# Optimization experiments

Hardware: AMD Instinct MI355X
Metric: run time of the kernel (lower is better)

Reference implementation:

```python
import jax, jax.numpy as jnp
import numpy as np
from jax import lax

H, W = 14, 14          # spatial input_size
K = 6                  # mask_size (square)
ST = 2                 # mask_stride
_xs = np.arange(0, H - K + 1, ST)   # mask/window positions; (H-K)%ST==0 so grid matches avg_pool2d
M = len(_xs)
# pairwise rectangle-intersection coordinates between mask R1 (index a) and window W2 (index b)
_lo = np.maximum(_xs[:, None], _xs[None, :])                       # [M,M]
_hi = np.maximum(np.minimum(_xs[:, None] + K, _xs[None, :] + K), _lo)  # [M,M], clamped (empty -> zero area)


def setup_inputs() -> dict:
    key = jax.random.key(0)
    x = jax.random.normal(key, (32, 1000, H, W), dtype=jnp.float32)
    return {"x": x}


def _forward(x):
    B, C = x.shape[0], x.shape[1]
    total = jnp.sum(x, axis=(2, 3))  # [B,C]  == unmasked_logits
    # window sums == avg_pool2d(divisor_override=1); also equals sum over each mask region R1
    winsum = lax.reduce_window(x, 0.0, lax.add, (1, 1, K, K), (1, 1, ST, ST), 'VALID')  # [B,C,M,M]
    one_mask_logits = total[:, :, None, None] - winsum                # [B,C,M,M]
    one_mask_pred = jnp.argmax(one_mask_logits, axis=1)               # [B,M,M]
    pred = jnp.argmax(total, axis=1)                                  # [B]
    disagree = one_mask_pred != pred[:, None, None]                   # [B,M,M]

    # summed-area table for O(1) rectangle sums (zero-padded)
    sat = jnp.pad(jnp.cumsum(jnp.cumsum(x, axis=2), axis=3), ((0, 0), (0, 0), (1, 0), (1, 0)))
    xhi = _hi[:, None, :, None]; xlo = _lo[:, None, :, None]          # depend on (i, k)
    yhi = _hi[None, :, None, :]; ylo = _lo[None, :, None, :]          # depend on (j, l)
    # sum of x over R1(i,j) ∩ W2(k,l): [B,C,M,M,M,M]
    overlap = (sat[:, :, xhi, yhi] - sat[:, :, xlo, yhi]
               - sat[:, :, xhi, ylo] + sat[:, :, xlo, ylo])

    # two-mask logits: total - sum(R1) - sum(W2) + sum(R1 ∩ W2)
    two = (total[:, :, None, None, None, None]
           - winsum[:, :, :, :, None, None]
           - winsum[:, :, None, None, :, :]
           + overlap)                                                 # [B,C,M,M,M,M]
    two_pred = jnp.argmax(two, axis=1)                                # [B,M,M,M,M]

    # a disagreer (i,j) is confirmed if ALL second-mask preds equal its one-mask pred
    agree = jnp.all(two_pred == one_mask_pred[:, :, :, None, None], axis=(3, 4))  # [B,M,M]
    cand = (disagree & agree).reshape(B, -1)                          # row-major (i,j) order
    first = jnp.argmax(cand, axis=1)                                  # first confirmed disagreer
    new_pred = jnp.take_along_axis(one_mask_pred.reshape(B, -1), first[:, None], axis=1)[:, 0]
    pred = jnp.where(jnp.any(cand, axis=1), new_pred, pred)
    return pred, one_mask_logits


def reference(x):
    pred, _ = _forward(x)
    return pred
```

## Files before the change

kernel.cpp:

```cpp
#include <hip/hip_runtime.h>


#define NC 1000
#define NBC 32000
#define CHUNKS 4
#define CLEN 250
#define NG 14
#define MAXST 26

__host__ __device__ constexpr int tri_off(int p) { return p * 25 - p * (p - 1) / 2; }

__device__ __forceinline__ unsigned fkey(float v) {
    unsigned u = __float_as_uint(v);
    return u ^ (unsigned)(((int)u >> 31) | 0x80000000);
}

__global__ __launch_bounds__(256) void satA(const float* __restrict__ x,
                                            float* __restrict__ Sws) {
    __shared__ float lx[64 * 197];
    const int tid = threadIdx.x;
    const int blk = blockIdx.x;
    const float4* x4 = reinterpret_cast<const float4*>(x) + (size_t)blk * 3136;
#pragma unroll
    for (int it = 0; it < 13; ++it) {
        int f = it * 256 + tid;
        if (f < 3136) {
            float4 v = x4[f];
            int img = f / 49;
            int off = f - img * 49;
            float* d = &lx[img * 197 + off * 4];
            d[0] = v.x; d[1] = v.y; d[2] = v.z; d[3] = v.w;
        }
    }
    __syncthreads();
    if (tid < 64) {
        const float* im = &lx[tid * 197];
        float S[8][8];
#pragma unroll
        for (int c = 0; c < 8; ++c) S[0][c] = 0.f;
        float colacc[7];
#pragma unroll
        for (int c = 0; c < 7; ++c) colacc[c] = 0.f;
#pragma unroll
        for (int r = 0; r < 7; ++r) {
            float rowf[28];
#pragma unroll
            for (int j = 0; j < 28; ++j) rowf[j] = im[r * 28 + j];
            S[r + 1][0] = 0.f;
            float run = 0.f;
#pragma unroll
            for (int c = 0; c < 7; ++c) {
                float blk2 = rowf[2 * c] + rowf[2 * c + 1] + rowf[14 + 2 * c] + rowf[14 + 2 * c + 1];
                colacc[c] += blk2;
                run += colacc[c];
                S[r + 1][c + 1] = run;
            }
        }
        const int bc = blk * 64 + tid;
#pragma unroll
        for (int k = 0; k < 64; ++k)
            Sws[(size_t)k * NBC + bc] = S[k >> 3][k & 7];
    }
}

#define WSUM(i, j) (S[((i)+3)*8+((j)+3)] - S[(i)*8+((j)+3)] - S[((i)+3)*8+(j)] + S[(i)*8+(j)])

template <int G>
__device__ __forceinline__ void procB(const float* __restrict__ Sws, int b, int chunk,
                                      unsigned long long* __restrict__ part,
                                      unsigned* __restrict__ kv, unsigned* __restrict__ kc) {
    const int tid = threadIdx.x;
    const int c = chunk * CLEN + tid;
    const bool act = (tid < CLEN);

    float S[64];
    if (act) {
        const int base = b * NC + c;
#pragma unroll
        for (int k = 0; k < 64; ++k) S[k] = Sws[k * NBC + base];
    } else {
#pragma unroll
        for (int k = 0; k < 64; ++k) S[k] = 0.f;
    }
    const float total = S[63];
    constexpr int NST = (G == 13) ? 26 : 25;

#pragma unroll
    for (int ph = 0; ph < 2; ++ph) {
        const int lo = ph * 13;
        const int cnt = (NST - lo) < 13 ? (NST - lo) : 13;
        if (act) {
#pragma unroll
            for (int i = 0; i < 13; ++i) {
                const int sl = lo + i;
                if (sl < NST) {
                    float v;
                    if constexpr (G == 13) {
                        v = (sl < 25) ? (total - WSUM(sl / 5, sl % 5)) : total;
                    } else {
                        const int pid = G * 25 + sl;
                        int p = 0;
                        while (tri_off(p + 1) <= pid) ++p;
                        const int q = p + (pid - tri_off(p));
                        const int p1 = p / 5, p2 = p % 5, q1 = q / 5, q2 = q % 5;
                        const int rlo = (p1 > q1 ? p1 : q1);
                        const int rmn = (p1 < q1 ? p1 : q1);
                        const int rhi = (rmn + 3 > rlo ? rmn + 3 : rlo);
                        const int clo = (p2 > q2 ? p2 : q2);
                        const int cmn = (p2 < q2 ? p2 : q2);
                        const int chi = (cmn + 3 > clo ? cmn + 3 : clo);
                        const float rect = S[rhi * 8 + chi] - S[rlo * 8 + chi]
                                         - S[rhi * 8 + clo] + S[rlo * 8 + clo];
                        v = ((total - WSUM(p1, p2)) - WSUM(q1, q2)) + rect;
                    }
                    kv[tid * 13 + i] = fkey(v);
                    kc[tid * 13 + i] = ~(unsigned)c;
                }
            }
        } else {
#pragma unroll
            for (int i = 0; i < 13; ++i) { kv[tid * 13 + i] = 0u; kc[tid * 13 + i] = 0u; }
        }
        __syncthreads();
        if (tid < 208) {
            const int s = tid >> 4, seg = tid & 15;
            if (s < cnt) {
                unsigned bk = 0u, bc2 = 0u;
#pragma unroll
                for (int i = 0; i < 16; ++i) {
                    const int row = seg * 16 + i;
                    unsigned k2 = kv[row * 13 + s], c2 = kc[row * 13 + s];
                    if (k2 > bk || (k2 == bk && c2 > bc2)) { bk = k2; bc2 = c2; }
                }
#pragma unroll
                for (int off = 1; off < 16; off <<= 1) {
                    unsigned ok = __shfl_xor(bk, off, 16);
                    unsigned oc = __shfl_xor(bc2, off, 16);
                    if (ok > bk || (ok == bk && oc > bc2)) { bk = ok; bc2 = oc; }
                }
                if (seg == 0)
                    part[((b * NG + G) * CHUNKS + chunk) * MAXST + lo + s] =
                        ((unsigned long long)bk << 32) | bc2;
            }
        }
        __syncthreads();
    }
}

__global__ __launch_bounds__(256) void kernB(const float* __restrict__ Sws,
                                             unsigned long long* __restrict__ part) {
    __shared__ unsigned kv[256 * 13];
    __shared__ unsigned kc[256 * 13];
    const int b = blockIdx.x / 56;
    const int r = blockIdx.x % 56;
    const int g = r >> 2;
    const int chunk = r & 3;
#define CASE_G(T) case T: procB<T>(Sws, b, chunk, part, kv, kc); break;
    switch (g) {
        CASE_G(0) CASE_G(1) CASE_G(2) CASE_G(3) CASE_G(4) CASE_G(5) CASE_G(6)
        CASE_G(7) CASE_G(8) CASE_G(9) CASE_G(10) CASE_G(11) CASE_G(12) CASE_G(13)
    }
#undef CASE_G
}

__global__ __launch_bounds__(64) void kernC(const unsigned long long* __restrict__ part,
                                            int* __restrict__ out) {
    const int b = blockIdx.x;
    const int t = threadIdx.x;
    auto mrg = [&](int g, int s) {
        unsigned long long m = 0ull;
#pragma unroll
        for (int ch = 0; ch < CHUNKS; ++ch) {
            unsigned long long v = part[((b * NG + g) * CHUNKS + ch) * MAXST + s];
            if (v > m) m = v;
        }
        return m;
    };
    const unsigned long long predk = mrg(13, 25);
    const int pred = (int)(~(unsigned)predk);

    int p1 = 0;
    bool ag = false;
    if (t < 25) {
        const unsigned long long p1k = mrg(13, t);
        const unsigned p1idx = (unsigned)p1k;
        p1 = (int)(~p1idx);
        ag = true;
        for (int j = 0; j < 25; ++j) {
            const int a = t < j ? t : j;
            const int bb = t < j ? j : t;
            const int pid = tri_off(a) + (bb - a);
            const unsigned long long fk = mrg(pid / 25, pid % 25);
            ag = ag && ((unsigned)fk == p1idx);
        }
    }
    const bool cand = (t < 25) && ag && (p1 != pred);
    const unsigned long long mask = __ballot(cand);
    int ans = pred;
    if (mask) {
        const int first = __ffsll((unsigned long long)mask) - 1;
        ans = __shfl(p1, first, 64);
    }
    if (t == 0) out[b] = ans;
}

extern "C" void kernel_launch(void* const* d_in, const int* in_sizes, int n_in,
                              void* d_out, int out_size, void* d_ws, size_t ws_size,
                              hipStream_t stream) {
    const float* x = (const float*)d_in[0];
    int* out = (int*)d_out;

    float* Sws = (float*)d_ws;
    unsigned long long* part =
        (unsigned long long*)((char*)d_ws + (size_t)64 * NBC * 4);

    satA<<<NBC / 64, 256, 0, stream>>>(x, Sws);
    kernB<<<32 * NG * CHUNKS, 256, 0, stream>>>(Sws, part);
    kernC<<<32, 64, 0, stream>>>(part, out);
}
```

Baseline: 103.7 us.

## Compute all mask pairs per wave with DPP argmax reductions instead of LDS

kernB now assigns each wave 64 classes and has every thread evaluate all 351 two-mask and one-mask logits from registers. Per-statistic argmax across the wave uses DPP max, readlane and ballot rather than shared-memory key arrays with block syncs. Each wave writes 351 partial results, and kernC merges 16 chunks through LDS before the agreement check. This removes redundant S loads across 14 group blocks and LDS traffic, at the cost of serialized per-wave reductions and only 256 blocks of 128 threads. The last chunk starts at class 936 and overlaps the previous one, which does not change the max.

```diff
diff --git a/kernel.cpp b/kernel.cpp
--- a/kernel.cpp
+++ b/kernel.cpp
@@ -3,17 +3,10 @@
 
 #define NC 1000
 #define NBC 32000
-#define CHUNKS 4
-#define CLEN 250
-#define NG 14
-#define MAXST 26
+#define NCH 16
+#define PSTRIDE 384
 
 __host__ __device__ constexpr int tri_off(int p) { return p * 25 - p * (p - 1) / 2; }
-
-__device__ __forceinline__ unsigned fkey(float v) {
-    unsigned u = __float_as_uint(v);
-    return u ^ (unsigned)(((int)u >> 31) | 0x80000000);
-}
 
 __global__ __launch_bounds__(256) void satA(const float* __restrict__ x,
                                             float* __restrict__ Sws) {
@@ -63,145 +56,128 @@
     }
 }
 
-#define WSUM(i, j) (S[((i)+3)*8+((j)+3)] - S[(i)*8+((j)+3)] - S[((i)+3)*8+(j)] + S[(i)*8+(j)])
+template <int CTRL>
+__device__ __forceinline__ float dppmax(float v) {
+    int o = __builtin_amdgcn_update_dpp(__float_as_int(v), __float_as_int(v),
+                                        CTRL, 0xF, 0xF, false);
+    return fmaxf(v, __int_as_float(o));
+}
 
-template <int G>
-__device__ __forceinline__ void procB(const float* __restrict__ Sws, int b, int chunk,
-                                      unsigned long long* __restrict__ part,
-                                      unsigned* __restrict__ kv, unsigned* __restrict__ kc) {
+__global__ __launch_bounds__(128) void kernB(const float* __restrict__ Sws,
+                                             unsigned long long* __restrict__ part) {
     const int tid = threadIdx.x;
-    const int c = chunk * CLEN + tid;
-    const bool act = (tid < CLEN);
+    const int lane = tid & 63;
+    const int b = blockIdx.x >> 3;
+    const int wc = ((blockIdx.x & 7) << 1) + (tid >> 6);
+    const int c0 = (wc == 15) ? 936 : wc * 64;
+    const int c = c0 + lane;
 
     float S[64];
-    if (act) {
-        const int base = b * NC + c;
 #pragma unroll
-        for (int k = 0; k < 64; ++k) S[k] = Sws[k * NBC + base];
-    } else {
+    for (int k = 0; k < 64; ++k)
+        S[k] = Sws[(size_t)k * NBC + b * NC + c];
+    const float total = S[63];
+
+    float w_[25], lt[25];
 #pragma unroll
-        for (int k = 0; k < 64; ++k) S[k] = 0.f;
+    for (int p1 = 0; p1 < 5; ++p1)
+#pragma unroll
+        for (int p2 = 0; p2 < 5; ++p2) {
+            float ww = ((S[(p1 + 3) * 8 + (p2 + 3)] - S[p1 * 8 + (p2 + 3)])
+                        - S[(p1 + 3) * 8 + p2]) + S[p1 * 8 + p2];
+            w_[p1 * 5 + p2] = ww;
+            lt[p1 * 5 + p2] = total - ww;
+        }
+
+    int rs_lo[6], rs_hi[6];
+#pragma unroll
+    for (int j = 0; j < 6; ++j) { rs_lo[j] = 0; rs_hi[j] = 0; }
+
+#define EMIT(VAL, SID)                                                          \
+    {                                                                           \
+        float _v = (VAL);                                                       \
+        float _m = _v;                                                          \
+        _m = dppmax<0x111>(_m); _m = dppmax<0x112>(_m);                         \
+        _m = dppmax<0x114>(_m); _m = dppmax<0x118>(_m);                         \
+        _m = dppmax<0x142>(_m); _m = dppmax<0x143>(_m);                         \
+        int _mb = __builtin_amdgcn_readlane(__float_as_int(_m), 63);            \
+        unsigned long long _eq = __ballot(__float_as_int(_v) == _mb);           \
+        int _off = __ffsll(_eq) - 1;                                            \
+        unsigned _cw = (unsigned)(c0 + _off);                                   \
+        unsigned _u = (unsigned)_mb;                                            \
+        unsigned _fk = _u ^ (unsigned)(((int)_u >> 31) | 0x80000000);           \
+        if (lane == ((SID) & 63)) {                                             \
+            rs_lo[(SID) >> 6] = (int)~_cw;                                      \
+            rs_hi[(SID) >> 6] = (int)_fk;                                       \
+        }                                                                       \
     }
-    const float total = S[63];
-    constexpr int NST = (G == 13) ? 26 : 25;
 
 #pragma unroll
-    for (int ph = 0; ph < 2; ++ph) {
-        const int lo = ph * 13;
-        const int cnt = (NST - lo) < 13 ? (NST - lo) : 13;
-        if (act) {
+    for (int p = 0; p < 25; ++p) {
 #pragma unroll
-            for (int i = 0; i < 13; ++i) {
-                const int sl = lo + i;
-                if (sl < NST) {
-                    float v;
-                    if constexpr (G == 13) {
-                        v = (sl < 25) ? (total - WSUM(sl / 5, sl % 5)) : total;
-                    } else {
-                        const int pid = G * 25 + sl;
-                        int p = 0;
-                        while (tri_off(p + 1) <= pid) ++p;
-                        const int q = p + (pid - tri_off(p));
-                        const int p1 = p / 5, p2 = p % 5, q1 = q / 5, q2 = q % 5;
-                        const int rlo = (p1 > q1 ? p1 : q1);
-                        const int rmn = (p1 < q1 ? p1 : q1);
-                        const int rhi = (rmn + 3 > rlo ? rmn + 3 : rlo);
-                        const int clo = (p2 > q2 ? p2 : q2);
-                        const int cmn = (p2 < q2 ? p2 : q2);
-                        const int chi = (cmn + 3 > clo ? cmn + 3 : clo);
-                        const float rect = S[rhi * 8 + chi] - S[rlo * 8 + chi]
-                                         - S[rhi * 8 + clo] + S[rlo * 8 + clo];
-                        v = ((total - WSUM(p1, p2)) - WSUM(q1, q2)) + rect;
-                    }
-                    kv[tid * 13 + i] = fkey(v);
-                    kc[tid * 13 + i] = ~(unsigned)c;
-                }
-            }
-        } else {
+        for (int q = 0; q < 25; ++q) {
+            if (q < p) continue;
+            const int p1 = p / 5, p2 = p % 5, q1 = q / 5, q2 = q % 5;
+            const int rlo = (p1 > q1 ? p1 : q1);
+            const int rmn = (p1 < q1 ? p1 : q1);
+            const int rhi = (rmn + 3 > rlo ? rmn + 3 : rlo);
+            const int clo = (p2 > q2 ? p2 : q2);
+            const int cmn = (p2 < q2 ? p2 : q2);
+            const int chi = (cmn + 3 > clo ? cmn + 3 : clo);
+            const float rect = ((S[rhi * 8 + chi] - S[rlo * 8 + chi])
+                                - S[rhi * 8 + clo]) + S[rlo * 8 + clo];
+            const float v = (lt[p] - w_[q]) + rect;
+            EMIT(v, tri_off(p) + (q - p));
+        }
+    }
 #pragma unroll
-            for (int i = 0; i < 13; ++i) { kv[tid * 13 + i] = 0u; kc[tid * 13 + i] = 0u; }
-        }
-        __syncthreads();
-        if (tid < 208) {
-            const int s = tid >> 4, seg = tid & 15;
-            if (s < cnt) {
-                unsigned bk = 0u, bc2 = 0u;
+    for (int i = 0; i < 25; ++i) EMIT(lt[i], 325 + i);
+    EMIT(total, 350);
+#undef EMIT
+
+    unsigned long long* dst = part + (size_t)(b * NCH + wc) * PSTRIDE + lane;
 #pragma unroll
-                for (int i = 0; i < 16; ++i) {
-                    const int row = seg * 16 + i;
-                    unsigned k2 = kv[row * 13 + s], c2 = kc[row * 13 + s];
-                    if (k2 > bk || (k2 == bk && c2 > bc2)) { bk = k2; bc2 = c2; }
-                }
-#pragma unroll
-                for (int off = 1; off < 16; off <<= 1) {
-                    unsigned ok = __shfl_xor(bk, off, 16);
-                    unsigned oc = __shfl_xor(bc2, off, 16);
-                    if (ok > bk || (ok == bk && oc > bc2)) { bk = ok; bc2 = oc; }
-                }
-                if (seg == 0)
-                    part[((b * NG + G) * CHUNKS + chunk) * MAXST + lo + s] =
-                        ((unsigned long long)bk << 32) | bc2;
-            }
-        }
-        __syncthreads();
-    }
+    for (int j = 0; j < 6; ++j)
+        dst[j * 64] = ((unsigned long long)(unsigned)rs_hi[j] << 32)
+                      | (unsigned)rs_lo[j];
 }
 
-__global__ __launch_bounds__(256) void kernB(const float* __restrict__ Sws,
-                                             unsigned long long* __restrict__ part) {
-    __shared__ unsigned kv[256 * 13];
-    __shared__ unsigned kc[256 * 13];
-    const int b = blockIdx.x / 56;
-    const int r = blockIdx.x % 56;
-    const int g = r >> 2;
-    const int chunk = r & 3;
-#define CASE_G(T) case T: procB<T>(Sws, b, chunk, part, kv, kc); break;
-    switch (g) {
-        CASE_G(0) CASE_G(1) CASE_G(2) CASE_G(3) CASE_G(4) CASE_G(5) CASE_G(6)
-        CASE_G(7) CASE_G(8) CASE_G(9) CASE_G(10) CASE_G(11) CASE_G(12) CASE_G(13)
-    }
-#undef CASE_G
-}
-
-__global__ __launch_bounds__(64) void kernC(const unsigned long long* __restrict__ part,
-                                            int* __restrict__ out) {
+__global__ __launch_bounds__(128) void kernC(const unsigned long long* __restrict__ part,
+                                             int* __restrict__ out) {
+    __shared__ unsigned long long mg[352];
     const int b = blockIdx.x;
     const int t = threadIdx.x;
-    auto mrg = [&](int g, int s) {
+    for (int s = t; s < 352; s += 128) {
         unsigned long long m = 0ull;
 #pragma unroll
-        for (int ch = 0; ch < CHUNKS; ++ch) {
-            unsigned long long v = part[((b * NG + g) * CHUNKS + ch) * MAXST + s];
+        for (int wc = 0; wc < NCH; ++wc) {
+            unsigned long long v = part[(size_t)(b * NCH + wc) * PSTRIDE + s];
             if (v > m) m = v;
         }
-        return m;
-    };
-    const unsigned long long predk = mrg(13, 25);
-    const int pred = (int)(~(unsigned)predk);
-
-    int p1 = 0;
-    bool ag = false;
-    if (t < 25) {
-        const unsigned long long p1k = mrg(13, t);
-        const unsigned p1idx = (unsigned)p1k;
-        p1 = (int)(~p1idx);
-        ag = true;
-        for (int j = 0; j < 25; ++j) {
-            const int a = t < j ? t : j;
-            const int bb = t < j ? j : t;
-            const int pid = tri_off(a) + (bb - a);
-            const unsigned long long fk = mrg(pid / 25, pid % 25);
-            ag = ag && ((unsigned)fk == p1idx);
+        mg[s] = m;
+    }
+    __syncthreads();
+    if (t < 64) {
+        const unsigned predidx = (unsigned)mg[350];
+        const int pred = (int)~predidx;
+        bool cand = false;
+        int p1 = 0;
+        if (t < 25) {
+            const unsigned p1i = (unsigned)mg[325 + t];
+            p1 = (int)~p1i;
+            bool ag = true;
+            for (int j = 0; j < 25; ++j) {
+                const int a = t < j ? t : j;
+                const int q = t < j ? j : t;
+                ag = ag && ((unsigned)mg[tri_off(a) + (q - a)] == p1i);
+            }
+            cand = ag && (p1 != pred);
         }
+        const unsigned long long mask = __ballot(cand);
+        int ans = pred;
+        if (mask) ans = __shfl(p1, __ffsll(mask) - 1, 64);
+        if (t == 0) out[b] = ans;
     }
-    const bool cand = (t < 25) && ag && (p1 != pred);
-    const unsigned long long mask = __ballot(cand);
-    int ans = pred;
-    if (mask) {
-        const int first = __ffsll((unsigned long long)mask) - 1;
-        ans = __shfl(p1, first, 64);
-    }
-    if (t == 0) out[b] = ans;
 }
 
 extern "C" void kernel_launch(void* const* d_in, const int* in_sizes, int n_in,
@@ -215,6 +191,6 @@
         (unsigned long long*)((char*)d_ws + (size_t)64 * NBC * 4);
 
     satA<<<NBC / 64, 256, 0, stream>>>(x, Sws);
-    kernB<<<32 * NG * CHUNKS, 256, 0, stream>>>(Sws, part);
-    kernC<<<32, 64, 0, stream>>>(part, out);
+    kernB<<<256, 128, 0, stream>>>(Sws, part);
+    kernC<<<32, 128, 0, stream>>>(part, out);
 }
```

Result: slower. 119.7 us (+15.5%).
